# Performance work log

Hardware: AMD Instinct MI355X
Metric: run time of the kernel (lower is better)

The kernel has to match this reference:

```python
import jax, jax.numpy as jnp
import numpy as np

N = 50000
E = 800000
IN_FEATS = 256
NUM_HEADS = 4
OUT_FEATS = 64
NUM_ETYPES = 8
ALPHA = 100.0
NEG_SLOPE_ATTN = 0.2   # self.leaky_relu
NEG_SLOPE_EW = 0.01    # nn.LeakyReLU() default, applied to edge weights


def leaky_relu(x, slope):
    return jnp.where(x >= 0, x, slope * x)


def setup_inputs() -> dict:
    key = jax.random.key(0)
    ks = jax.random.split(key, 8)
    feat = jax.random.normal(ks[0], (N, IN_FEATS), dtype=jnp.float32)
    src = jax.random.randint(ks[1], (E,), 0, N, dtype=jnp.int32)
    dst = jax.random.randint(ks[2], (E,), 0, N, dtype=jnp.int32)
    # etypes are 1-indexed in the original code (edge_weight[edge_feats - 1])
    edge_feats = jax.random.randint(ks[3], (E,), 1, NUM_ETYPES + 1, dtype=jnp.int32)
    # parameters (xavier-normal-ish init for weights; edge_weight = 1/alpha)
    fc_w = jax.random.normal(ks[4], (NUM_HEADS * OUT_FEATS, IN_FEATS), dtype=jnp.float32) * 0.05
    attn_l = jax.random.normal(ks[5], (1, NUM_HEADS, OUT_FEATS), dtype=jnp.float32) * 0.1
    attn_r = jax.random.normal(ks[6], (1, NUM_HEADS, OUT_FEATS), dtype=jnp.float32) * 0.1
    edge_weight = jnp.full((NUM_ETYPES, NUM_HEADS), 1.0 / ALPHA, dtype=jnp.float32)
    return {"feat": feat, "src": src, "dst": dst, "edge_feats": edge_feats,
            "fc_w": fc_w, "attn_l": attn_l, "attn_r": attn_r, "edge_weight": edge_weight}


def reference(feat, src, dst, edge_feats, fc_w, attn_l, attn_r, edge_weight):
    # feat: [N, F_in] -> ft: [N, H, D]
    ft = (feat @ fc_w.T).reshape(-1, NUM_HEADS, OUT_FEATS)
    el = jnp.einsum('nhd,ohd->nh', ft, attn_l)  # [N, H]
    er = jnp.einsum('nhd,ohd->nh', ft, attn_r)  # [N, H]
    # edge-type weights (1-indexed), scaled & leaky-relu'd
    ew = leaky_relu(edge_weight * ALPHA, NEG_SLOPE_EW)  # [T, H]
    ee = ew[edge_feats - 1]                              # [E, H]
    # per-edge logits: u_add_v, times edge weight, leaky relu
    e = leaky_relu((el[src] + er[dst]) * ee, NEG_SLOPE_ATTN)  # [E, H]
    # edge softmax grouped by destination node
    emax = jax.ops.segment_max(e, dst, num_segments=N)        # [N, H]
    ex = jnp.exp(e - emax[dst])
    denom = jax.ops.segment_sum(ex, dst, num_segments=N)      # [N, H]
    a = ex / denom[dst]                                        # [E, H]
    # weighted scatter-sum: sum over edges of a * ft[src]
    msg = ft[src] * a[:, :, None]                              # [E, H, D]
    rst = jax.ops.segment_sum(msg, dst, num_segments=N)       # [N, H, D]
    return rst
```

## Files before the change

### kernel.cpp

```cpp
#include <hip/hip_runtime.h>
#include <hip/hip_bf16.h>


#define NF 256
#define HD 256
#define NH 4

typedef __attribute__((ext_vector_type(8))) short short8;
typedef __attribute__((ext_vector_type(4))) float f32x4;

static __device__ __forceinline__ unsigned short f2bf(float f) {
  unsigned int u = __float_as_uint(f);
  u += 0x7FFFu + ((u >> 16) & 1u);
  return (unsigned short)(u >> 16);
}
static __device__ __forceinline__ float bf2f(unsigned short s) {
  return __uint_as_float(((unsigned int)s) << 16);
}
static __device__ __forceinline__ unsigned pkbf(float a, float b) {
  __hip_bfloat162 h = __float22bfloat162_rn(make_float2(a, b));
  return *(unsigned*)&h;
}

__global__ __launch_bounds__(256) void hist_cvt_rank_k(
    const int* __restrict__ dst, int* __restrict__ cursor,
    int* __restrict__ rank, const float* __restrict__ w,
    unsigned short* __restrict__ o, int e) {
  int i = blockIdx.x * 256 + threadIdx.x;
  if (i < 16384) {
    float4 v = ((const float4*)w)[i];
    ((uint2*)o)[i] = make_uint2(pkbf(v.x, v.y), pkbf(v.z, v.w));
  }
  if (i < e) rank[i] = atomicAdd(&cursor[dst[i]], 1);
}

__global__ __launch_bounds__(1024) void scan_k(const int* __restrict__ cursor,
                                               int* __restrict__ offs, int n) {
  __shared__ int wtot[16];
  __shared__ int wexcl[16];
  __shared__ int ctot;
  int tid = threadIdx.x, lane = tid & 63, wid = tid >> 6;
  int carry = 0;
  int nchunk = (n + 8191) >> 13;
  for (int c = 0; c < nchunk; ++c) {
    int base = (c << 13) + tid * 8;
    int v[8];
    if (base + 8 <= n) {
      int4 a = *(const int4*)(cursor + base);
      int4 b = *(const int4*)(cursor + base + 4);
      v[0] = a.x; v[1] = a.y; v[2] = a.z; v[3] = a.w;
      v[4] = b.x; v[5] = b.y; v[6] = b.z; v[7] = b.w;
    } else {
#pragma unroll
      for (int j = 0; j < 8; ++j) v[j] = (base + j < n) ? cursor[base + j] : 0;
    }
    int p[8]; int run = 0;
#pragma unroll
    for (int j = 0; j < 8; ++j) { run += v[j]; p[j] = run; }
    int incl = run;
#pragma unroll
    for (int off = 1; off < 64; off <<= 1) {
      int t = __shfl_up(incl, off);
      if (lane >= off) incl += t;
    }
    if (lane == 63) wtot[wid] = incl;
    __syncthreads();
    if (wid == 0 && lane < 16) {
      int wv = wtot[lane]; int wi = wv;
#pragma unroll
      for (int off = 1; off < 16; off <<= 1) {
        int t = __shfl_up(wi, off);
        if (lane >= off) wi += t;
      }
      wexcl[lane] = wi - wv;
      if (lane == 15) ctot = wi;
    }
    __syncthreads();
    int ebase = carry + wexcl[wid] + (incl - run);
#pragma unroll
    for (int j = 0; j < 8; ++j) {
      int i = base + j;
      if (i < n) offs[i] = ebase + p[j] - v[j];
    }
    carry += ctot;
    __syncthreads();
  }
  if (tid == 0) offs[n] = carry;
}

__global__ __launch_bounds__(256) void gemm_k(
    const float* __restrict__ feat, const unsigned short* __restrict__ fcb,
    const float* __restrict__ attn_l, const float* __restrict__ attn_r,
    unsigned short* __restrict__ ftb, float* __restrict__ el,
    float* __restrict__ er, int n) {
  __shared__ short aF[4 * 2 * 64 * 8];
  __shared__ short bF[16 * 2 * 64 * 8];
  int tid = threadIdx.x;
  int lane = tid & 63, w = tid >> 6;
  int row0 = blockIdx.x * 64;

  f32x4 acc[4][4];
#pragma unroll
  for (int i = 0; i < 4; ++i)
#pragma unroll
    for (int j = 0; j < 4; ++j) acc[i][j] = (f32x4){0.f, 0.f, 0.f, 0.f};

  int ar = tid >> 2, ak = (tid & 3) << 4;
  int arow = row0 + ar; if (arow >= n) arow = n - 1;
  const float* ap = feat + (size_t)arow * NF + ak;
  int am = ar & 15, art = ar >> 4;
  int s0 = ak >> 5, q0 = (ak >> 3) & 3;
  int s1 = (ak + 8) >> 5, q1 = ((ak + 8) >> 3) & 3;
  short* aw0 = &aF[(((art * 2 + s0) * 64) + q0 * 16 + am) * 8];
  short* aw1 = &aF[(((art * 2 + s1) * 64) + q1 * 16 + am) * 8];

  const unsigned short* bp = fcb + (size_t)tid * NF;
  int bn = tid & 15, bcg = tid >> 4;

  for (int k0 = 0; k0 < NF; k0 += 64) {
    float4 f0 = *(const float4*)(ap + k0);
    float4 f1 = *(const float4*)(ap + k0 + 4);
    float4 f2 = *(const float4*)(ap + k0 + 8);
    float4 f3 = *(const float4*)(ap + k0 + 12);
    uint4 oa = make_uint4(pkbf(f0.x, f0.y), pkbf(f0.z, f0.w),
                          pkbf(f1.x, f1.y), pkbf(f1.z, f1.w));
    uint4 ob = make_uint4(pkbf(f2.x, f2.y), pkbf(f2.z, f2.w),
                          pkbf(f3.x, f3.y), pkbf(f3.z, f3.w));
    *(uint4*)aw0 = oa;
    *(uint4*)aw1 = ob;
#pragma unroll
    for (int o8 = 0; o8 < 8; ++o8) {
      short8 bv = *(const short8*)(bp + k0 + o8 * 8);
      int bs = o8 >> 2, bq = o8 & 3;
      *(short8*)&bF[(((bcg * 2 + bs) * 64) + bq * 16 + bn) * 8] = bv;
    }
    __syncthreads();
#pragma unroll
    for (int s = 0; s < 2; ++s) {
      short8 af[4], bfr[4];
#pragma unroll
      for (int rt = 0; rt < 4; ++rt)
        af[rt] = *(const short8*)&aF[(((rt * 2 + s) * 64) + lane) * 8];
#pragma unroll
      for (int ct = 0; ct < 4; ++ct)
        bfr[ct] = *(const short8*)&bF[((((w * 4 + ct) * 2 + s) * 64) + lane) * 8];
#pragma unroll
      for (int rt = 0; rt < 4; ++rt)
#pragma unroll
        for (int ct = 0; ct < 4; ++ct)
          acc[rt][ct] = __builtin_amdgcn_mfma_f32_16x16x32_bf16(
              af[rt], bfr[ct], acc[rt][ct], 0, 0, 0);
    }
    __syncthreads();
  }

  int ln = lane & 15, lq = lane >> 4;
  float al4[4], ar4[4];
#pragma unroll
  for (int ct = 0; ct < 4; ++ct) {
    al4[ct] = attn_l[w * 64 + ct * 16 + ln];
    ar4[ct] = attn_r[w * 64 + ct * 16 + ln];
  }
#pragma unroll
  for (int rt = 0; rt < 4; ++rt) {
#pragma unroll
    for (int r = 0; r < 4; ++r) {
      float pl = 0.f, pr = 0.f;
#pragma unroll
      for (int ct = 0; ct < 4; ++ct) {
        float v = acc[rt][ct][r];
        pl += v * al4[ct]; pr += v * ar4[ct];
      }
#pragma unroll
      for (int off = 1; off <= 8; off <<= 1) {
        pl += __shfl_xor(pl, off);
        pr += __shfl_xor(pr, off);
      }
      int row = row0 + rt * 16 + lq * 4 + r;
      if (row < n) {
        if (ln == 0) { el[row * NH + w] = pl; er[row * NH + w] = pr; }
        unsigned short* fr = ftb + (size_t)row * HD + w * 64 + ln;
#pragma unroll
        for (int ct = 0; ct < 4; ++ct) fr[ct * 16] = f2bf(acc[rt][ct][r]);
      }
    }
  }
}

__global__ __launch_bounds__(256) void scatter4_k(
    const int* __restrict__ src, const int* __restrict__ dst,
    const int* __restrict__ efeats, const int* __restrict__ rank,
    const int* __restrict__ offs, const float* __restrict__ el,
    const float* __restrict__ er, const float* __restrict__ ewt,
    int* __restrict__ srcs_g, float4* __restrict__ exq, int e) {
  __shared__ float ew_s[32];
  if (threadIdx.x < 32) {
    float v = ewt[threadIdx.x] * 100.0f;
    ew_s[threadIdx.x] = (v >= 0.f) ? v : 0.01f * v;
  }
  __syncthreads();
  int i = blockIdx.x * 256 + threadIdx.x;
  if (i >= e) return;
  int d = dst[i], s = src[i], t = efeats[i] - 1;
  int p = offs[d] + rank[i];
  float4 elv = *(const float4*)(el + (size_t)s * 4);
  float4 erv = *(const float4*)(er + (size_t)d * 4);
  const float* ew = &ew_s[t * 4];
  float x0 = (elv.x + erv.x) * ew[0]; x0 = (x0 >= 0.f) ? x0 : 0.2f * x0;
  float x1 = (elv.y + erv.y) * ew[1]; x1 = (x1 >= 0.f) ? x1 : 0.2f * x1;
  float x2 = (elv.z + erv.z) * ew[2]; x2 = (x2 >= 0.f) ? x2 : 0.2f * x2;
  float x3 = (elv.w + erv.w) * ew[3]; x3 = (x3 >= 0.f) ? x3 : 0.2f * x3;
  exq[p] = make_float4(__expf(x0), __expf(x1), __expf(x2), __expf(x3));
  srcs_g[p] = s;
}

__global__ __launch_bounds__(256) void agg2_k(
    const unsigned short* __restrict__ ftb, const int* __restrict__ srcs_g,
    const float4* __restrict__ exq, const int* __restrict__ offs,
    float* __restrict__ out, int n) {
  int node = blockIdx.x * 4 + (threadIdx.x >> 6);
  int lane = threadIdx.x & 63;
  if (node >= n) return;
  int start = offs[node];
  int deg = offs[node + 1] - start;
  float o0 = 0.f, o1 = 0.f, o2 = 0.f, o3 = 0.f;
  if (deg > 0) {
    float s0 = 0.f, s1 = 0.f, s2 = 0.f, s3 = 0.f;
    for (int i = lane; i < deg; i += 64) {
      float4 q = exq[(size_t)start + i];
      s0 += q.x; s1 += q.y; s2 += q.z; s3 += q.w;
    }
#pragma unroll
    for (int off = 1; off < 64; off <<= 1) {
      s0 += __shfl_xor(s0, off);
      s1 += __shfl_xor(s1, off);
      s2 += __shfl_xor(s2, off);
      s3 += __shfl_xor(s3, off);
    }
    int hl = lane >> 4;
    float sh = (hl == 0) ? s0 : (hl == 1) ? s1 : (hl == 2) ? s2 : s3;
    float rs = 1.0f / sh;
    const float* exs = (const float*)exq;
    const unsigned short* fb = ftb + (size_t)lane * 4;
    const int* sg = srcs_g + start;
    long b4 = (long)start * 4 + hl;
    int i = 0;
    for (; i + 8 <= deg; i += 8) {
      int sA = sg[i],     sB = sg[i + 1], sC = sg[i + 2], sD = sg[i + 3];
      int sE = sg[i + 4], sF = sg[i + 5], sG = sg[i + 6], sH = sg[i + 7];
      ushort4 fA = *(const ushort4*)(fb + (size_t)sA * HD);
      ushort4 fB = *(const ushort4*)(fb + (size_t)sB * HD);
      ushort4 fC = *(const ushort4*)(fb + (size_t)sC * HD);
      ushort4 fD = *(const ushort4*)(fb + (size_t)sD * HD);
      ushort4 fE = *(const ushort4*)(fb + (size_t)sE * HD);
      ushort4 fF = *(const ushort4*)(fb + (size_t)sF * HD);
      ushort4 fG = *(const ushort4*)(fb + (size_t)sG * HD);
      ushort4 fH = *(const ushort4*)(fb + (size_t)sH * HD);
      float wA = exs[b4 + (long)i * 4]       * rs;
      float wB = exs[b4 + (long)(i + 1) * 4] * rs;
      float wC = exs[b4 + (long)(i + 2) * 4] * rs;
      float wD = exs[b4 + (long)(i + 3) * 4] * rs;
      float wE = exs[b4 + (long)(i + 4) * 4] * rs;
      float wF = exs[b4 + (long)(i + 5) * 4] * rs;
      float wG = exs[b4 + (long)(i + 6) * 4] * rs;
      float wH = exs[b4 + (long)(i + 7) * 4] * rs;
      o0 = fmaf(wA, bf2f(fA.x), o0); o1 = fmaf(wA, bf2f(fA.y), o1);
      o2 = fmaf(wA, bf2f(fA.z), o2); o3 = fmaf(wA, bf2f(fA.w), o3);
      o0 = fmaf(wB, bf2f(fB.x), o0); o1 = fmaf(wB, bf2f(fB.y), o1);
      o2 = fmaf(wB, bf2f(fB.z), o2); o3 = fmaf(wB, bf2f(fB.w), o3);
      o0 = fmaf(wC, bf2f(fC.x), o0); o1 = fmaf(wC, bf2f(fC.y), o1);
      o2 = fmaf(wC, bf2f(fC.z), o2); o3 = fmaf(wC, bf2f(fC.w), o3);
      o0 = fmaf(wD, bf2f(fD.x), o0); o1 = fmaf(wD, bf2f(fD.y), o1);
      o2 = fmaf(wD, bf2f(fD.z), o2); o3 = fmaf(wD, bf2f(fD.w), o3);
      o0 = fmaf(wE, bf2f(fE.x), o0); o1 = fmaf(wE, bf2f(fE.y), o1);
      o2 = fmaf(wE, bf2f(fE.z), o2); o3 = fmaf(wE, bf2f(fE.w), o3);
      o0 = fmaf(wF, bf2f(fF.x), o0); o1 = fmaf(wF, bf2f(fF.y), o1);
      o2 = fmaf(wF, bf2f(fF.z), o2); o3 = fmaf(wF, bf2f(fF.w), o3);
      o0 = fmaf(wG, bf2f(fG.x), o0); o1 = fmaf(wG, bf2f(fG.y), o1);
      o2 = fmaf(wG, bf2f(fG.z), o2); o3 = fmaf(wG, bf2f(fG.w), o3);
      o0 = fmaf(wH, bf2f(fH.x), o0); o1 = fmaf(wH, bf2f(fH.y), o1);
      o2 = fmaf(wH, bf2f(fH.z), o2); o3 = fmaf(wH, bf2f(fH.w), o3);
    }
    for (; i < deg; ++i) {
      int sA = sg[i];
      float wA = exs[b4 + (long)i * 4] * rs;
      ushort4 fA = *(const ushort4*)(fb + (size_t)sA * HD);
      o0 = fmaf(wA, bf2f(fA.x), o0); o1 = fmaf(wA, bf2f(fA.y), o1);
      o2 = fmaf(wA, bf2f(fA.z), o2); o3 = fmaf(wA, bf2f(fA.w), o3);
    }
  }
  *(float4*)(out + (size_t)node * HD + lane * 4) = make_float4(o0, o1, o2, o3);
}

extern "C" void kernel_launch(void* const* d_in, const int* in_sizes, int n_in,
                              void* d_out, int out_size, void* d_ws, size_t ws_size,
                              hipStream_t stream) {
  const float* feat   = (const float*)d_in[0];
  const int*   src    = (const int*)d_in[1];
  const int*   dst    = (const int*)d_in[2];
  const int*   efeats = (const int*)d_in[3];
  const float* fc_w   = (const float*)d_in[4];
  const float* attn_l = (const float*)d_in[5];
  const float* attn_r = (const float*)d_in[6];
  const float* ewt    = (const float*)d_in[7];
  float* out = (float*)d_out;

  int N = in_sizes[0] / NF;
  int E = in_sizes[1];

  char* ws = (char*)d_ws;
  size_t off = 0;
  unsigned short* fcb = (unsigned short*)(ws + off); off += (size_t)NF * HD * 2;
  unsigned short* ftb = (unsigned short*)(ws + off); off += (size_t)N * HD * 2;
  float* el  = (float*)(ws + off);  off += (size_t)N * NH * 4;
  float* er  = (float*)(ws + off);  off += (size_t)N * NH * 4;
  int* offs  = (int*)(ws + off);    off += ((size_t)N + 16) * 4;
  int* cursor = (int*)(ws + off);   off += (size_t)N * 4;
  int* rank  = (int*)(ws + off);    off += (size_t)E * 4;
  int* srcs_g = (int*)(ws + off);   off += (size_t)E * 4;
  float4* exq = (float4*)(ws + off); off += (size_t)E * 16;

  hipMemsetAsync(cursor, 0, (size_t)N * 4, stream);
  hist_cvt_rank_k<<<(E + 255) / 256, 256, 0, stream>>>(dst, cursor, rank, fc_w, fcb, E);
  scan_k<<<1, 1024, 0, stream>>>(cursor, offs, N);
  gemm_k<<<(N + 63) / 64, 256, 0, stream>>>(feat, fcb, attn_l, attn_r, ftb, el, er, N);
  scatter4_k<<<(E + 255) / 256, 256, 0, stream>>>(src, dst, efeats, rank, offs,
                                                  el, er, ewt, srcs_g, exq, E);
  agg2_k<<<(N + 3) / 4, 256, 0, stream>>>(ftb, srcs_g, exq, offs, out, N);
}
```

Baseline: 299.6 us.

## Move edge logit and softmax computation into the aggregation kernel with packed CSR entries

Edge scores are no longer computed per edge and stored as float4 exp values. A pack kernel now places each edge into CSR order through a second atomic cursor pass, writing src and etype packed into one int. The aggregation kernel then gathers el per source, computes exp on the fly, accumulates the softmax denominator alongside the weighted sum, and normalizes at the end. This drops the rank array, the exq buffer and the separate denominator pass. The cost is recomputed exp per lane and an extra el gather in the inner loop. Like the old code it skips max subtraction, and edge order within a node is now nondeterministic.

```diff
diff --git a/kernel.cpp b/kernel.cpp
--- a/kernel.cpp
+++ b/kernel.cpp
@@ -21,20 +21,24 @@
   __hip_bfloat162 h = __float22bfloat162_rn(make_float2(a, b));
   return *(unsigned*)&h;
 }
-
-__global__ __launch_bounds__(256) void hist_cvt_rank_k(
+static __device__ __forceinline__ float wcalc(float sum, float ew) {
+  float x = sum * ew;
+  x = (x >= 0.f) ? x : 0.2f * x;
+  return __expf(x);
+}
+
+__global__ __launch_bounds__(256) void hist_cvt_k(
     const int* __restrict__ dst, int* __restrict__ cursor,
-    int* __restrict__ rank, const float* __restrict__ w,
-    unsigned short* __restrict__ o, int e) {
+    const float* __restrict__ w, unsigned short* __restrict__ o, int e) {
   int i = blockIdx.x * 256 + threadIdx.x;
   if (i < 16384) {
     float4 v = ((const float4*)w)[i];
     ((uint2*)o)[i] = make_uint2(pkbf(v.x, v.y), pkbf(v.z, v.w));
   }
-  if (i < e) rank[i] = atomicAdd(&cursor[dst[i]], 1);
-}
-
-__global__ __launch_bounds__(1024) void scan_k(const int* __restrict__ cursor,
+  if (i < e) atomicAdd(&cursor[dst[i]], 1);
+}
+
+__global__ __launch_bounds__(1024) void scan_k(int* __restrict__ cursor,
                                                int* __restrict__ offs, int n) {
   __shared__ int wtot[16];
   __shared__ int wexcl[16];
@@ -80,7 +84,11 @@
 #pragma unroll
     for (int j = 0; j < 8; ++j) {
       int i = base + j;
-      if (i < n) offs[i] = ebase + p[j] - v[j];
+      if (i < n) {
+        int ex = ebase + p[j] - v[j];
+        offs[i] = ex;
+        cursor[i] = ex;
+      }
     }
     carry += ctot;
     __syncthreads();
@@ -187,37 +195,28 @@
   }
 }
 
-__global__ __launch_bounds__(256) void scatter4_k(
+__global__ __launch_bounds__(256) void pack_k(
     const int* __restrict__ src, const int* __restrict__ dst,
-    const int* __restrict__ efeats, const int* __restrict__ rank,
-    const int* __restrict__ offs, const float* __restrict__ el,
-    const float* __restrict__ er, const float* __restrict__ ewt,
-    int* __restrict__ srcs_g, float4* __restrict__ exq, int e) {
+    const int* __restrict__ efeats, int* __restrict__ cursor,
+    int* __restrict__ pk, int e) {
+  int i = blockIdx.x * 256 + threadIdx.x;
+  if (i >= e) return;
+  int d = dst[i];
+  int p = atomicAdd(&cursor[d], 1);
+  pk[p] = src[i] | ((efeats[i] - 1) << 17);
+}
+
+__global__ __launch_bounds__(256) void agg3_k(
+    const unsigned short* __restrict__ ftb, const int* __restrict__ pk,
+    const float* __restrict__ el, const float* __restrict__ er,
+    const float* __restrict__ ewt, const int* __restrict__ offs,
+    float* __restrict__ out, int n) {
   __shared__ float ew_s[32];
   if (threadIdx.x < 32) {
     float v = ewt[threadIdx.x] * 100.0f;
     ew_s[threadIdx.x] = (v >= 0.f) ? v : 0.01f * v;
   }
   __syncthreads();
-  int i = blockIdx.x * 256 + threadIdx.x;
-  if (i >= e) return;
-  int d = dst[i], s = src[i], t = efeats[i] - 1;
-  int p = offs[d] + rank[i];
-  float4 elv = *(const float4*)(el + (size_t)s * 4);
-  float4 erv = *(const float4*)(er + (size_t)d * 4);
-  const float* ew = &ew_s[t * 4];
-  float x0 = (elv.x + erv.x) * ew[0]; x0 = (x0 >= 0.f) ? x0 : 0.2f * x0;
-  float x1 = (elv.y + erv.y) * ew[1]; x1 = (x1 >= 0.f) ? x1 : 0.2f * x1;
-  float x2 = (elv.z + erv.z) * ew[2]; x2 = (x2 >= 0.f) ? x2 : 0.2f * x2;
-  float x3 = (elv.w + erv.w) * ew[3]; x3 = (x3 >= 0.f) ? x3 : 0.2f * x3;
-  exq[p] = make_float4(__expf(x0), __expf(x1), __expf(x2), __expf(x3));
-  srcs_g[p] = s;
-}
-
-__global__ __launch_bounds__(256) void agg2_k(
-    const unsigned short* __restrict__ ftb, const int* __restrict__ srcs_g,
-    const float4* __restrict__ exq, const int* __restrict__ offs,
-    float* __restrict__ out, int n) {
   int node = blockIdx.x * 4 + (threadIdx.x >> 6);
   int lane = threadIdx.x & 63;
   if (node >= n) return;
@@ -225,29 +224,26 @@
   int deg = offs[node + 1] - start;
   float o0 = 0.f, o1 = 0.f, o2 = 0.f, o3 = 0.f;
   if (deg > 0) {
-    float s0 = 0.f, s1 = 0.f, s2 = 0.f, s3 = 0.f;
-    for (int i = lane; i < deg; i += 64) {
-      float4 q = exq[(size_t)start + i];
-      s0 += q.x; s1 += q.y; s2 += q.z; s3 += q.w;
-    }
-#pragma unroll
-    for (int off = 1; off < 64; off <<= 1) {
-      s0 += __shfl_xor(s0, off);
-      s1 += __shfl_xor(s1, off);
-      s2 += __shfl_xor(s2, off);
-      s3 += __shfl_xor(s3, off);
-    }
     int hl = lane >> 4;
-    float sh = (hl == 0) ? s0 : (hl == 1) ? s1 : (hl == 2) ? s2 : s3;
-    float rs = 1.0f / sh;
-    const float* exs = (const float*)exq;
+    float er_h = er[(size_t)node * NH + hl];
     const unsigned short* fb = ftb + (size_t)lane * 4;
-    const int* sg = srcs_g + start;
-    long b4 = (long)start * 4 + hl;
+    const float* elh = el + hl;
+    const int* pg = pk + start;
+    float ss = 0.f;
     int i = 0;
     for (; i + 8 <= deg; i += 8) {
-      int sA = sg[i],     sB = sg[i + 1], sC = sg[i + 2], sD = sg[i + 3];
-      int sE = sg[i + 4], sF = sg[i + 5], sG = sg[i + 6], sH = sg[i + 7];
+      int4 pa = *(const int4*)(pg + i);
+      int4 pb = *(const int4*)(pg + i + 4);
+      int sA = pa.x & 0x1FFFF, tA = pa.x >> 17;
+      int sB = pa.y & 0x1FFFF, tB = pa.y >> 17;
+      int sC = pa.z & 0x1FFFF, tC = pa.z >> 17;
+      int sD = pa.w & 0x1FFFF, tD = pa.w >> 17;
+      int sE = pb.x & 0x1FFFF, tE = pb.x >> 17;
+      int sF = pb.y & 0x1FFFF, tF = pb.y >> 17;
+      int sG = pb.z & 0x1FFFF, tG = pb.z >> 17;
+      int sH = pb.w & 0x1FFFF, tH = pb.w >> 17;
+      float eA = elh[sA * NH], eB = elh[sB * NH], eC = elh[sC * NH], eD = elh[sD * NH];
+      float eE = elh[sE * NH], eF = elh[sF * NH], eG = elh[sG * NH], eH = elh[sH * NH];
       ushort4 fA = *(const ushort4*)(fb + (size_t)sA * HD);
       ushort4 fB = *(const ushort4*)(fb + (size_t)sB * HD);
       ushort4 fC = *(const ushort4*)(fb + (size_t)sC * HD);
@@ -256,14 +252,15 @@
       ushort4 fF = *(const ushort4*)(fb + (size_t)sF * HD);
       ushort4 fG = *(const ushort4*)(fb + (size_t)sG * HD);
       ushort4 fH = *(const ushort4*)(fb + (size_t)sH * HD);
-      float wA = exs[b4 + (long)i * 4]       * rs;
-      float wB = exs[b4 + (long)(i + 1) * 4] * rs;
-      float wC = exs[b4 + (long)(i + 2) * 4] * rs;
-      float wD = exs[b4 + (long)(i + 3) * 4] * rs;
-      float wE = exs[b4 + (long)(i + 4) * 4] * rs;
-      float wF = exs[b4 + (long)(i + 5) * 4] * rs;
-      float wG = exs[b4 + (long)(i + 6) * 4] * rs;
-      float wH = exs[b4 + (long)(i + 7) * 4] * rs;
+      float wA = wcalc(eA + er_h, ew_s[tA * NH + hl]);
+      float wB = wcalc(eB + er_h, ew_s[tB * NH + hl]);
+      float wC = wcalc(eC + er_h, ew_s[tC * NH + hl]);
+      float wD = wcalc(eD + er_h, ew_s[tD * NH + hl]);
+      float wE = wcalc(eE + er_h, ew_s[tE * NH + hl]);
+      float wF = wcalc(eF + er_h, ew_s[tF * NH + hl]);
+      float wG = wcalc(eG + er_h, ew_s[tG * NH + hl]);
+      float wH = wcalc(eH + er_h, ew_s[tH * NH + hl]);
+      ss += ((wA + wB) + (wC + wD)) + ((wE + wF) + (wG + wH));
       o0 = fmaf(wA, bf2f(fA.x), o0); o1 = fmaf(wA, bf2f(fA.y), o1);
       o2 = fmaf(wA, bf2f(fA.z), o2); o3 = fmaf(wA, bf2f(fA.w), o3);
       o0 = fmaf(wB, bf2f(fB.x), o0); o1 = fmaf(wB, bf2f(fB.y), o1);
@@ -282,12 +279,17 @@
       o2 = fmaf(wH, bf2f(fH.z), o2); o3 = fmaf(wH, bf2f(fH.w), o3);
     }
     for (; i < deg; ++i) {
-      int sA = sg[i];
-      float wA = exs[b4 + (long)i * 4] * rs;
+      int pv = pg[i];
+      int sA = pv & 0x1FFFF, tA = pv >> 17;
+      float eA = elh[sA * NH];
       ushort4 fA = *(const ushort4*)(fb + (size_t)sA * HD);
+      float wA = wcalc(eA + er_h, ew_s[tA * NH + hl]);
+      ss += wA;
       o0 = fmaf(wA, bf2f(fA.x), o0); o1 = fmaf(wA, bf2f(fA.y), o1);
       o2 = fmaf(wA, bf2f(fA.z), o2); o3 = fmaf(wA, bf2f(fA.w), o3);
     }
+    float rs = 1.0f / ss;
+    o0 *= rs; o1 *= rs; o2 *= rs; o3 *= rs;
   }
   *(float4*)(out + (size_t)node * HD + lane * 4) = make_float4(o0, o1, o2, o3);
 }
@@ -316,15 +318,12 @@
   float* er  = (float*)(ws + off);  off += (size_t)N * NH * 4;
   int* offs  = (int*)(ws + off);    off += ((size_t)N + 16) * 4;
   int* cursor = (int*)(ws + off);   off += (size_t)N * 4;
-  int* rank  = (int*)(ws + off);    off += (size_t)E * 4;
-  int* srcs_g = (int*)(ws + off);   off += (size_t)E * 4;
-  float4* exq = (float4*)(ws + off); off += (size_t)E * 16;
+  int* pk    = (int*)(ws + off);    off += (size_t)E * 4;
 
   hipMemsetAsync(cursor, 0, (size_t)N * 4, stream);
-  hist_cvt_rank_k<<<(E + 255) / 256, 256, 0, stream>>>(dst, cursor, rank, fc_w, fcb, E);
+  hist_cvt_k<<<(E + 255) / 256, 256, 0, stream>>>(dst, cursor, fc_w, fcb, E);
   scan_k<<<1, 1024, 0, stream>>>(cursor, offs, N);
   gemm_k<<<(N + 63) / 64, 256, 0, stream>>>(feat, fcb, attn_l, attn_r, ftb, el, er, N);
-  scatter4_k<<<(E + 255) / 256, 256, 0, stream>>>(src, dst, efeats, rank, offs,
-                                                  el, er, ewt, srcs_g, exq, E);
-  agg2_k<<<(N + 3) / 4, 256, 0, stream>>>(ftb, srcs_g, exq, offs, out, N);
-}
+  pack_k<<<(E + 255) / 256, 256, 0, stream>>>(src, dst, efeats, cursor, pk, E);
+  agg3_k<<<(N + 3) / 4, 256, 0, stream>>>(ftb, pk, el, er, ewt, offs, out, N);
+}
```

Measured after the change: 335.6 us. +12.0%, slower.
